# Kernel tuning notes

Measured on AMD Instinct MI355X. Metric: run time of the kernel, lower is better.

The kernel has to match this reference:

```python
import jax, jax.numpy as jnp
import numpy as np

N_NODES = 50000
N_EDGES = 800000
D_IN = 128
D_HID = 128
D_OUT = 128
EPS = 0.1  # GINConv eps


def setup_inputs() -> dict:
    key = jax.random.key(0)
    k = jax.random.split(key, 8)
    scale = 1.0 / np.sqrt(D_IN)
    return {
        "x": jax.random.normal(k[0], (N_NODES, D_IN), dtype=jnp.float32),
        "edge_index": jax.random.randint(k[1], (2, N_EDGES), 0, N_NODES, dtype=jnp.int64),
        "edge_weight": jax.random.uniform(k[2], (N_EDGES,), dtype=jnp.float32),
        "W1a": jax.random.normal(k[3], (D_IN, D_HID), dtype=jnp.float32) * scale,
        "W1b": jax.random.normal(k[4], (D_HID, D_HID), dtype=jnpp.float32) if False else jax.random.normal(k[4], (D_HID, D_HID), dtype=jnp.float32) * scale,
        "W2a": jax.random.normal(k[5], (D_HID, D_HID), dtype=jnp.float32) * scale,
        "W2b": jax.random.normal(k[6], (D_HID, D_OUT), dtype=jnp.float32) * scale,
    }


def _gin_conv(h, src, dst, ew, Wa, Wb, n_nodes):
    # edge-weighted neighbor sum: aggr[i] = sum_{(j->i)} w_ji * h[j]
    msg = ew[:, None] * h[src]                       # [E, d]
    aggr = jax.ops.segment_sum(msg, dst, num_segments=n_nodes)  # [N, d]
    z = (1.0 + EPS) * h + aggr                       # GIN update
    # 2-layer bias-free MLP: lin -> relu -> lin
    return jnp.maximum(z @ Wa, 0.0) @ Wb


def reference(x, edge_index, edge_weight, W1a, W1b, W2a, W2b):
    src, dst = edge_index[0], edge_index[1]
    n = x.shape[0]
    h = _gin_conv(x, src, dst, edge_weight, W1a, W1b, n)
    h = jnp.maximum(h, 0.0)  # relu between convs; dropout is identity in eval
    h = _gin_conv(h, src, dst, edge_weight, W2a, W2b, n)
    return h
```

## Files before the change

kernel.cpp:

```cpp
#include <hip/hip_runtime.h>
#include <hip/hip_fp16.h>

#define D 128
#define N_NODES 50000
#define EPSP1 1.1f

#define NPB 256
#define NBUCK 196
#define CAP 5120
#define P1E 2048
#define TS 136

typedef __attribute__((ext_vector_type(8))) short short8;
typedef __attribute__((ext_vector_type(4))) float f32x4;

__device__ __forceinline__ unsigned short f2bf(float f) {
    unsigned u = __float_as_uint(f);
    u += 0x7FFF + ((u >> 16) & 1);
    return (unsigned short)(u >> 16);
}
__device__ __forceinline__ float bf2f(unsigned short h) {
    return __uint_as_float(((unsigned)h) << 16);
}

__global__ __launch_bounds__(256) void pass1_all(
    const int* __restrict__ src, const int* __restrict__ dst,
    const float* __restrict__ ew, int* __restrict__ gcnt,
    uint2* __restrict__ gstage, int ne, int nb1,
    const float* __restrict__ x, unsigned short* __restrict__ hb,
    int n4, int ncvt,
    const float* __restrict__ W1a, const float* __restrict__ W1b,
    const float* __restrict__ W2a, const float* __restrict__ W2b,
    unsigned short* __restrict__ wp)
{
    __shared__ int bcnt[NBUCK];
    __shared__ int goff[NBUCK];
    int tid = threadIdx.x;
    int bid = blockIdx.x;

    if (bid < nb1) {
        if (tid < NBUCK) bcnt[tid] = 0;
        __syncthreads();
        int e0 = bid * P1E;
        int   rank[8];
        int   buck[8];
        uint2 pay[8];
#pragma unroll
        for (int j = 0; j < 8; ++j) {
            int e = e0 + j * 256 + tid;
            buck[j] = -1;
            if (e < ne) {
                int d_ = dst[e];
                int b  = d_ >> 8;
                int dl = d_ & 255;
                pay[j].x = (unsigned)(src[e] & 0xFFFF) | ((unsigned)dl << 16);
                pay[j].y = (unsigned)__half_as_ushort(__float2half_rn(ew[e]));
                rank[j]  = atomicAdd(&bcnt[b], 1);
                buck[j]  = b;
            }
        }
        __syncthreads();
        if (tid < NBUCK && bcnt[tid] > 0)
            goff[tid] = atomicAdd(&gcnt[tid], bcnt[tid]);
        __syncthreads();
#pragma unroll
        for (int j = 0; j < 8; ++j) {
            if (buck[j] >= 0) {
                int pos = goff[buck[j]] + rank[j];
                if (pos < CAP)
                    gstage[(size_t)buck[j] * CAP + pos] = pay[j];
            }
        }
    } else if (bid < nb1 + ncvt) {
        int base = (bid - nb1) * 2048;
#pragma unroll
        for (int it = 0; it < 8; ++it) {
            int i = base + it * 256 + tid;
            if (i < n4) {
                float4 v = ((const float4*)x)[i];
                ushort4 o;
                o.x = f2bf(v.x); o.y = f2bf(v.y); o.z = f2bf(v.z); o.w = f2bf(v.w);
                ((ushort4*)hb)[i] = o;
            }
        }
    } else {
        int e2 = (bid - nb1 - ncvt) * 256 + tid;
        if (e2 < 8192) {
            int mat = e2 >> 11;
            int e   = e2 & 2047;
            const float* W = (mat == 0) ? W1a : (mat == 1) ? W1b : (mat == 2) ? W2a : W2b;
            unsigned short* Wp = wp + (size_t)mat * 16384;
            int col = e & 127;
            int kq  = e >> 7;
            short8 v;
#pragma unroll
            for (int j = 0; j < 8; ++j)
                v[j] = (short)f2bf(W[(size_t)(kq * 8 + j) * 128 + col]);
            ((short8*)Wp)[e] = v;
        }
    }
}

__global__ __launch_bounds__(512) void csr_build(
    const uint2* __restrict__ gstage, const int* __restrict__ gcnt,
    unsigned* __restrict__ epay, int* __restrict__ off)
{
    __shared__ int hist[NPB];
    __shared__ int scn[NPB];
    __shared__ int loc[NPB];
    __shared__ int wtot[8];
    __shared__ int base_s;
    __shared__ unsigned csr[CAP];

    int b = blockIdx.x;
    int t = threadIdx.x;
    int cnt = min(gcnt[b], CAP);

    if (t < NPB) hist[t] = 0;
    __syncthreads();

    uint2 ent[CAP / 512];
#pragma unroll
    for (int it = 0; it < CAP / 512; ++it) {
        int i = it * 512 + t;
        if (i < cnt) {
            ent[it] = gstage[(size_t)b * CAP + i];
            atomicAdd(&hist[(ent[it].x >> 16) & 255], 1);
        }
    }
    __syncthreads();

    int w = t >> 6, l = t & 63;
    if (w < 4) {
        int v = hist[w * 64 + l];
#pragma unroll
        for (int dd = 1; dd < 64; dd <<= 1) {
            int u = __shfl_up(v, dd, 64);
            if (l >= dd) v += u;
        }
        scn[w * 64 + l] = v;
        if (l == 63) wtot[w] = v;
    } else if (w == 4) {
        int v = 0;
        for (int i = l; i < NBUCK; i += 64)
            if (i < b) v += min(gcnt[i], CAP);
#pragma unroll
        for (int dd = 32; dd > 0; dd >>= 1) v += __shfl_down(v, dd, 64);
        if (l == 0) base_s = v;
    }
    __syncthreads();

    if (t < NPB) {
        int pre = 0;
#pragma unroll
        for (int j = 0; j < 3; ++j) if (j < w) pre += wtot[j];
        int incl = scn[t] + pre;
        int excl = incl - hist[t];
        int node = (b << 8) + t;
        if (node <= N_NODES) off[node] = base_s + excl;
        loc[t] = excl;
    }
    __syncthreads();

#pragma unroll
    for (int it = 0; it < CAP / 512; ++it) {
        int i = it * 512 + t;
        if (i < cnt) {
            int dl = (ent[it].x >> 16) & 255;
            int p = atomicAdd(&loc[dl], 1);
            csr[p] = (ent[it].x & 0xFFFF) | (ent[it].y << 16);
        }
    }
    __syncthreads();

    for (int i = t; i < cnt; i += 512)
        epay[base_s + i] = csr[i];
}

template<int RELU2, int OUT_F32>
__global__ __launch_bounds__(256, 8) void conv_fused(
    const unsigned short* __restrict__ h, const int* __restrict__ off,
    const unsigned* __restrict__ epay,
    const unsigned short* __restrict__ WpA,
    const unsigned short* __restrict__ WpB,
    void* __restrict__ outv, int n)
{
    __shared__ unsigned short t1[16 * TS];
    __shared__ unsigned short t2[16 * TS];

    int tid  = threadIdx.x;
    int wave = tid >> 6;
    int lane = tid & 63;
    int qtr  = lane >> 4;
    int sub  = lane & 15;
    int nb   = blockIdx.x * 16;

    const short8 zero8 = {0, 0, 0, 0, 0, 0, 0, 0};

    for (int nd = 0; nd < 4; ++nd) {
        int row  = wave * 4 + nd;
        int node = nb + row;
        float acc[8];
#pragma unroll
        for (int c = 0; c < 8; ++c) acc[c] = 0.f;

        if (node < n) {
            int beg = off[node];
            int end = off[node + 1];
            int i = beg;
            for (; i + 16 <= end; i += 16) {
                unsigned p0 = epay[i + qtr];
                unsigned p1 = epay[i + 4 + qtr];
                unsigned p2 = epay[i + 8 + qtr];
                unsigned p3 = epay[i + 12 + qtr];
                short8 v0 = ((const short8*)(h + (size_t)(p0 & 0xFFFF) * D))[sub];
                short8 v1 = ((const short8*)(h + (size_t)(p1 & 0xFFFF) * D))[sub];
                short8 v2 = ((const short8*)(h + (size_t)(p2 & 0xFFFF) * D))[sub];
                short8 v3 = ((const short8*)(h + (size_t)(p3 & 0xFFFF) * D))[sub];
                float w0 = __half2float(__ushort_as_half((unsigned short)(p0 >> 16)));
                float w1 = __half2float(__ushort_as_half((unsigned short)(p1 >> 16)));
                float w2 = __half2float(__ushort_as_half((unsigned short)(p2 >> 16)));
                float w3 = __half2float(__ushort_as_half((unsigned short)(p3 >> 16)));
#pragma unroll
                for (int c = 0; c < 8; ++c)
                    acc[c] += w0 * bf2f((unsigned short)v0[c]) + w1 * bf2f((unsigned short)v1[c])
                            + w2 * bf2f((unsigned short)v2[c]) + w3 * bf2f((unsigned short)v3[c]);
            }
            for (; i + 8 <= end; i += 8) {
                unsigned p0 = epay[i + qtr];
                unsigned p1 = epay[i + 4 + qtr];
                short8 v0 = ((const short8*)(h + (size_t)(p0 & 0xFFFF) * D))[sub];
                short8 v1 = ((const short8*)(h + (size_t)(p1 & 0xFFFF) * D))[sub];
                float w0 = __half2float(__ushort_as_half((unsigned short)(p0 >> 16)));
                float w1 = __half2float(__ushort_as_half((unsigned short)(p1 >> 16)));
#pragma unroll
                for (int c = 0; c < 8; ++c)
                    acc[c] += w0 * bf2f((unsigned short)v0[c]) + w1 * bf2f((unsigned short)v1[c]);
            }
            for (; i + qtr < end; i += 4) {
                unsigned p0 = epay[i + qtr];
                short8 v0 = ((const short8*)(h + (size_t)(p0 & 0xFFFF) * D))[sub];
                float w0 = __half2float(__ushort_as_half((unsigned short)(p0 >> 16)));
#pragma unroll
                for (int c = 0; c < 8; ++c)
                    acc[c] += w0 * bf2f((unsigned short)v0[c]);
            }
        }

#pragma unroll
        for (int c = 0; c < 8; ++c) {
            acc[c] += __shfl(acc[c], (lane + 32) & 63, 64);
            acc[c] += __shfl(acc[c], (lane + 16) & 63, 64);
        }

        if (qtr == 0) {
            short8 o;
            if (node < n) {
                short8 xv = ((const short8*)(h + (size_t)node * D))[sub];
#pragma unroll
                for (int c = 0; c < 8; ++c)
                    o[c] = (short)f2bf(acc[c] + EPSP1 * bf2f((unsigned short)xv[c]));
            } else {
                o = zero8;
            }
            *(short8*)&t1[row * TS + sub * 8] = o;
        }
    }
    __syncthreads();

    short8 a[4];
#pragma unroll
    for (int kk = 0; kk < 4; ++kk)
        a[kk] = *(const short8*)&t1[sub * TS + kk * 32 + qtr * 8];

    f32x4 acc2[2];
#pragma unroll
    for (int j = 0; j < 2; ++j) acc2[j] = (f32x4){0.f, 0.f, 0.f, 0.f};

#pragma unroll
    for (int j = 0; j < 2; ++j) {
        int cf = wave * 2 + j;
        short8 b[4];
#pragma unroll
        for (int kk = 0; kk < 4; ++kk)
            b[kk] = *(const short8*)(WpA + ((size_t)(kk * 4 + qtr) * 128 + cf * 16 + sub) * 8);
#pragma unroll
        for (int kk = 0; kk < 4; ++kk)
            acc2[j] = __builtin_amdgcn_mfma_f32_16x16x32_bf16(a[kk], b[kk], acc2[j], 0, 0, 0);
    }

#pragma unroll
    for (int j = 0; j < 2; ++j) {
        int cf = wave * 2 + j;
#pragma unroll
        for (int reg = 0; reg < 4; ++reg) {
            int row = qtr * 4 + reg;
            t2[row * TS + cf * 16 + sub] = f2bf(fmaxf(acc2[j][reg], 0.f));
        }
    }
    __syncthreads();

#pragma unroll
    for (int kk = 0; kk < 4; ++kk)
        a[kk] = *(const short8*)&t2[sub * TS + kk * 32 + qtr * 8];

#pragma unroll
    for (int j = 0; j < 2; ++j) acc2[j] = (f32x4){0.f, 0.f, 0.f, 0.f};

#pragma unroll
    for (int j = 0; j < 2; ++j) {
        int cf = wave * 2 + j;
        short8 b[4];
#pragma unroll
        for (int kk = 0; kk < 4; ++kk)
            b[kk] = *(const short8*)(WpB + ((size_t)(kk * 4 + qtr) * 128 + cf * 16 + sub) * 8);
#pragma unroll
        for (int kk = 0; kk < 4; ++kk)
            acc2[j] = __builtin_amdgcn_mfma_f32_16x16x32_bf16(a[kk], b[kk], acc2[j], 0, 0, 0);
    }

#pragma unroll
    for (int j = 0; j < 2; ++j) {
        int cf = wave * 2 + j;
#pragma unroll
        for (int reg = 0; reg < 4; ++reg) {
            int row = nb + qtr * 4 + reg;
            if (row < n) {
                float v = acc2[j][reg];
                if (RELU2) v = fmaxf(v, 0.f);
                int col = cf * 16 + sub;
                if (OUT_F32)
                    ((float*)outv)[(size_t)row * D + col] = v;
                else
                    ((unsigned short*)outv)[(size_t)row * D + col] = f2bf(v);
            }
        }
    }
}

extern "C" void kernel_launch(void* const* d_in, const int* in_sizes, int n_in,
                              void* d_out, int out_size, void* d_ws, size_t ws_size,
                              hipStream_t stream) {
    const float* x   = (const float*)d_in[0];
    const int*   ei  = (const int*)d_in[1];
    const float* ew  = (const float*)d_in[2];
    const float* W1a = (const float*)d_in[3];
    const float* W1b = (const float*)d_in[4];
    const float* W2a = (const float*)d_in[5];
    const float* W2b = (const float*)d_in[6];
    float* out = (float*)d_out;

    int n_edges = in_sizes[2];
    const int* src = ei;
    const int* dst = ei + n_edges;

    size_t node_elems = (size_t)N_NODES * D;
    unsigned short* hb = (unsigned short*)d_ws;
    unsigned short* zb = hb + node_elems;
    unsigned short* wp = zb + node_elems;
    unsigned* epay = (unsigned*)(wp + 4 * 16384);
    uint2*  gstage = (uint2*)(epay + n_edges);
    int*    gcnt   = (int*)(gstage + (size_t)NBUCK * CAP);
    int*    off    = gcnt + NBUCK;

    int nb1   = (n_edges + P1E - 1) / P1E;
    int n4    = (int)(node_elems / 4);
    int ncvt  = (n4 + 2047) / 2048;
    int npack = 32;
    int cgrid = (N_NODES + 15) / 16;

    hipMemsetAsync(gcnt, 0, NBUCK * sizeof(int), stream);

    pass1_all<<<nb1 + ncvt + npack, 256, 0, stream>>>(
        src, dst, ew, gcnt, gstage, n_edges, nb1,
        x, hb, n4, ncvt, W1a, W1b, W2a, W2b, wp);

    csr_build<<<NBUCK, 512, 0, stream>>>(gstage, gcnt, epay, off);

    unsigned short* wp0 = wp;
    unsigned short* wp1 = wp + 16384;
    unsigned short* wp2 = wp + 2 * 16384;
    unsigned short* wp3 = wp + 3 * 16384;

    conv_fused<1, 0><<<cgrid, 256, 0, stream>>>(hb, off, epay, wp0, wp1, zb, N_NODES);

    conv_fused<0, 1><<<cgrid, 256, 0, stream>>>(zb, off, epay, wp2, wp3, out, N_NODES);
}
```

Baseline: 187.8 us.

## Stage block edge lists in LDS and map one node per quarter-wave

The fused conv kernel now loads the 17 CSR offsets and the block's whole edge payload slice into shared memory once, then gives each quarter-wave one node to gather sequentially. Before, each wave walked four nodes in turn with the edges split across quarters, which needed a shuffle reduction per node. This removes the cross-lane reductions and the repeated global epay reads. The bucketing is also rescaled to 128 nodes per bucket with half-size pass-1 chunks, which gives more csr_build blocks and smaller per-bucket capacity, with a higher risk of overflowing CAP. Per-node load imbalance within a wave becomes possible, and a global fallback path is kept for blocks whose edge count exceeds the LDS buffer.

```diff
diff --git a/kernel.cpp b/kernel.cpp
--- a/kernel.cpp
+++ b/kernel.cpp
@@ -5,11 +5,12 @@
 #define N_NODES 50000
 #define EPSP1 1.1f
 
-#define NPB 256
-#define NBUCK 196
-#define CAP 5120
-#define P1E 2048
+#define NPB 128
+#define NBUCK 391
+#define CAP 2560
+#define P1E 1024
 #define TS 136
+#define ECAP 1024
 
 typedef __attribute__((ext_vector_type(8))) short short8;
 typedef __attribute__((ext_vector_type(4))) float f32x4;
@@ -39,20 +40,20 @@
     int bid = blockIdx.x;
 
     if (bid < nb1) {
-        if (tid < NBUCK) bcnt[tid] = 0;
+        for (int i = tid; i < NBUCK; i += 256) bcnt[i] = 0;
         __syncthreads();
         int e0 = bid * P1E;
-        int   rank[8];
-        int   buck[8];
-        uint2 pay[8];
-#pragma unroll
-        for (int j = 0; j < 8; ++j) {
+        int   rank[4];
+        int   buck[4];
+        uint2 pay[4];
+#pragma unroll
+        for (int j = 0; j < 4; ++j) {
             int e = e0 + j * 256 + tid;
             buck[j] = -1;
             if (e < ne) {
                 int d_ = dst[e];
-                int b  = d_ >> 8;
-                int dl = d_ & 255;
+                int b  = d_ >> 7;
+                int dl = d_ & 127;
                 pay[j].x = (unsigned)(src[e] & 0xFFFF) | ((unsigned)dl << 16);
                 pay[j].y = (unsigned)__half_as_ushort(__float2half_rn(ew[e]));
                 rank[j]  = atomicAdd(&bcnt[b], 1);
@@ -60,11 +61,11 @@
             }
         }
         __syncthreads();
-        if (tid < NBUCK && bcnt[tid] > 0)
-            goff[tid] = atomicAdd(&gcnt[tid], bcnt[tid]);
+        for (int i = tid; i < NBUCK; i += 256)
+            if (bcnt[i] > 0) goff[i] = atomicAdd(&gcnt[i], bcnt[i]);
         __syncthreads();
 #pragma unroll
-        for (int j = 0; j < 8; ++j) {
+        for (int j = 0; j < 4; ++j) {
             if (buck[j] >= 0) {
                 int pos = goff[buck[j]] + rank[j];
                 if (pos < CAP)
@@ -108,7 +109,7 @@
     __shared__ int hist[NPB];
     __shared__ int scn[NPB];
     __shared__ int loc[NPB];
-    __shared__ int wtot[8];
+    __shared__ int wtot[2];
     __shared__ int base_s;
     __shared__ unsigned csr[CAP];
 
@@ -131,7 +132,7 @@
     __syncthreads();
 
     int w = t >> 6, l = t & 63;
-    if (w < 4) {
+    if (w < 2) {
         int v = hist[w * 64 + l];
 #pragma unroll
         for (int dd = 1; dd < 64; dd <<= 1) {
@@ -140,7 +141,7 @@
         }
         scn[w * 64 + l] = v;
         if (l == 63) wtot[w] = v;
-    } else if (w == 4) {
+    } else if (w == 2) {
         int v = 0;
         for (int i = l; i < NBUCK; i += 64)
             if (i < b) v += min(gcnt[i], CAP);
@@ -151,12 +152,10 @@
     __syncthreads();
 
     if (t < NPB) {
-        int pre = 0;
-#pragma unroll
-        for (int j = 0; j < 3; ++j) if (j < w) pre += wtot[j];
+        int pre = (t >= 64) ? wtot[0] : 0;
         int incl = scn[t] + pre;
         int excl = incl - hist[t];
-        int node = (b << 8) + t;
+        int node = (b << 7) + t;
         if (node <= N_NODES) off[node] = base_s + excl;
         loc[t] = excl;
     }
@@ -175,6 +174,41 @@
 
     for (int i = t; i < cnt; i += 512)
         epay[base_s + i] = csr[i];
+}
+
+template<bool L>
+__device__ __forceinline__ void gather_node(
+    const unsigned short* __restrict__ h,
+    const unsigned* eLp, const unsigned* __restrict__ egp,
+    int lb, int le, int sub, float* acc)
+{
+    int i = lb;
+    for (; i + 4 <= le; i += 4) {
+        unsigned p0 = L ? eLp[i]     : egp[i];
+        unsigned p1 = L ? eLp[i + 1] : egp[i + 1];
+        unsigned p2 = L ? eLp[i + 2] : egp[i + 2];
+        unsigned p3 = L ? eLp[i + 3] : egp[i + 3];
+        short8 v0 = ((const short8*)(h + (size_t)(p0 & 0xFFFF) * D))[sub];
+        short8 v1 = ((const short8*)(h + (size_t)(p1 & 0xFFFF) * D))[sub];
+        short8 v2 = ((const short8*)(h + (size_t)(p2 & 0xFFFF) * D))[sub];
+        short8 v3 = ((const short8*)(h + (size_t)(p3 & 0xFFFF) * D))[sub];
+        float w0 = __half2float(__ushort_as_half((unsigned short)(p0 >> 16)));
+        float w1 = __half2float(__ushort_as_half((unsigned short)(p1 >> 16)));
+        float w2 = __half2float(__ushort_as_half((unsigned short)(p2 >> 16)));
+        float w3 = __half2float(__ushort_as_half((unsigned short)(p3 >> 16)));
+#pragma unroll
+        for (int c = 0; c < 8; ++c)
+            acc[c] += w0 * bf2f((unsigned short)v0[c]) + w1 * bf2f((unsigned short)v1[c])
+                    + w2 * bf2f((unsigned short)v2[c]) + w3 * bf2f((unsigned short)v3[c]);
+    }
+    for (; i < le; ++i) {
+        unsigned p0 = L ? eLp[i] : egp[i];
+        short8 v0 = ((const short8*)(h + (size_t)(p0 & 0xFFFF) * D))[sub];
+        float w0 = __half2float(__ushort_as_half((unsigned short)(p0 >> 16)));
+#pragma unroll
+        for (int c = 0; c < 8; ++c)
+            acc[c] += w0 * bf2f((unsigned short)v0[c]);
+    }
 }
 
 template<int RELU2, int OUT_F32>
@@ -187,6 +221,8 @@
 {
     __shared__ unsigned short t1[16 * TS];
     __shared__ unsigned short t2[16 * TS];
+    __shared__ unsigned eL[ECAP];
+    __shared__ int offs[17];
 
     int tid  = threadIdx.x;
     int wave = tid >> 6;
@@ -195,76 +231,40 @@
     int sub  = lane & 15;
     int nb   = blockIdx.x * 16;
 
-    const short8 zero8 = {0, 0, 0, 0, 0, 0, 0, 0};
-
-    for (int nd = 0; nd < 4; ++nd) {
-        int row  = wave * 4 + nd;
-        int node = nb + row;
-        float acc[8];
-#pragma unroll
-        for (int c = 0; c < 8; ++c) acc[c] = 0.f;
-
+    if (tid < 17) offs[tid] = off[min(nb + tid, n)];
+    __syncthreads();
+    int ebeg = offs[0];
+    int ecnt = offs[16] - ebeg;
+    int stg  = min(ecnt, ECAP);
+    for (int i = tid; i < stg; i += 256) eL[i] = epay[ebeg + i];
+    __syncthreads();
+
+    int row  = wave * 4 + qtr;
+    int node = nb + row;
+    int lb = offs[row]     - ebeg;
+    int le = offs[row + 1] - ebeg;
+
+    float acc[8];
+#pragma unroll
+    for (int c = 0; c < 8; ++c) acc[c] = 0.f;
+
+    if (ecnt <= ECAP)
+        gather_node<true >(h, eL, epay + ebeg, lb, le, sub, acc);
+    else
+        gather_node<false>(h, eL, epay + ebeg, lb, le, sub, acc);
+
+    {
+        const short8 zero8 = {0, 0, 0, 0, 0, 0, 0, 0};
+        short8 o;
         if (node < n) {
-            int beg = off[node];
-            int end = off[node + 1];
-            int i = beg;
-            for (; i + 16 <= end; i += 16) {
-                unsigned p0 = epay[i + qtr];
-                unsigned p1 = epay[i + 4 + qtr];
-                unsigned p2 = epay[i + 8 + qtr];
-                unsigned p3 = epay[i + 12 + qtr];
-                short8 v0 = ((const short8*)(h + (size_t)(p0 & 0xFFFF) * D))[sub];
-                short8 v1 = ((const short8*)(h + (size_t)(p1 & 0xFFFF) * D))[sub];
-                short8 v2 = ((const short8*)(h + (size_t)(p2 & 0xFFFF) * D))[sub];
-                short8 v3 = ((const short8*)(h + (size_t)(p3 & 0xFFFF) * D))[sub];
-                float w0 = __half2float(__ushort_as_half((unsigned short)(p0 >> 16)));
-                float w1 = __half2float(__ushort_as_half((unsigned short)(p1 >> 16)));
-                float w2 = __half2float(__ushort_as_half((unsigned short)(p2 >> 16)));
-                float w3 = __half2float(__ushort_as_half((unsigned short)(p3 >> 16)));
-#pragma unroll
-                for (int c = 0; c < 8; ++c)
-                    acc[c] += w0 * bf2f((unsigned short)v0[c]) + w1 * bf2f((unsigned short)v1[c])
-                            + w2 * bf2f((unsigned short)v2[c]) + w3 * bf2f((unsigned short)v3[c]);
-            }
-            for (; i + 8 <= end; i += 8) {
-                unsigned p0 = epay[i + qtr];
-                unsigned p1 = epay[i + 4 + qtr];
-                short8 v0 = ((const short8*)(h + (size_t)(p0 & 0xFFFF) * D))[sub];
-                short8 v1 = ((const short8*)(h + (size_t)(p1 & 0xFFFF) * D))[sub];
-                float w0 = __half2float(__ushort_as_half((unsigned short)(p0 >> 16)));
-                float w1 = __half2float(__ushort_as_half((unsigned short)(p1 >> 16)));
-#pragma unroll
-                for (int c = 0; c < 8; ++c)
-                    acc[c] += w0 * bf2f((unsigned short)v0[c]) + w1 * bf2f((unsigned short)v1[c]);
-            }
-            for (; i + qtr < end; i += 4) {
-                unsigned p0 = epay[i + qtr];
-                short8 v0 = ((const short8*)(h + (size_t)(p0 & 0xFFFF) * D))[sub];
-                float w0 = __half2float(__ushort_as_half((unsigned short)(p0 >> 16)));
-#pragma unroll
-                for (int c = 0; c < 8; ++c)
-                    acc[c] += w0 * bf2f((unsigned short)v0[c]);
-            }
-        }
-
-#pragma unroll
-        for (int c = 0; c < 8; ++c) {
-            acc[c] += __shfl(acc[c], (lane + 32) & 63, 64);
-            acc[c] += __shfl(acc[c], (lane + 16) & 63, 64);
-        }
-
-        if (qtr == 0) {
-            short8 o;
-            if (node < n) {
-                short8 xv = ((const short8*)(h + (size_t)node * D))[sub];
-#pragma unroll
-                for (int c = 0; c < 8; ++c)
-                    o[c] = (short)f2bf(acc[c] + EPSP1 * bf2f((unsigned short)xv[c]));
-            } else {
-                o = zero8;
-            }
-            *(short8*)&t1[row * TS + sub * 8] = o;
-        }
+            short8 xv = ((const short8*)(h + (size_t)node * D))[sub];
+#pragma unroll
+            for (int c = 0; c < 8; ++c)
+                o[c] = (short)f2bf(acc[c] + EPSP1 * bf2f((unsigned short)xv[c]));
+        } else {
+            o = zero8;
+        }
+        *(short8*)&t1[row * TS + sub * 8] = o;
     }
     __syncthreads();
 
@@ -294,8 +294,8 @@
         int cf = wave * 2 + j;
 #pragma unroll
         for (int reg = 0; reg < 4; ++reg) {
-            int row = qtr * 4 + reg;
-            t2[row * TS + cf * 16 + sub] = f2bf(fmaxf(acc2[j][reg], 0.f));
+            int r = qtr * 4 + reg;
+            t2[r * TS + cf * 16 + sub] = f2bf(fmaxf(acc2[j][reg], 0.f));
         }
     }
     __syncthreads();
@@ -324,15 +324,15 @@
         int cf = wave * 2 + j;
 #pragma unroll
         for (int reg = 0; reg < 4; ++reg) {
-            int row = nb + qtr * 4 + reg;
-            if (row < n) {
+            int r = nb + qtr * 4 + reg;
+            if (r < n) {
                 float v = acc2[j][reg];
                 if (RELU2) v = fmaxf(v, 0.f);
                 int col = cf * 16 + sub;
                 if (OUT_F32)
-                    ((float*)outv)[(size_t)row * D + col] = v;
+                    ((float*)outv)[(size_t)r * D + col] = v;
                 else
-                    ((unsigned short*)outv)[(size_t)row * D + col] = f2bf(v);
+                    ((unsigned short*)outv)[(size_t)r * D + col] = f2bf(v);
             }
         }
     }
```

New measurement: 190.6 us. About the same (+1.5%).
